# Kernel tuning notes

Measured on AMD Instinct MI355X. Metric: run time of the kernel, lower is better.

## Reference

```python
import jax, jax.numpy as jnp
import numpy as np

B, C, H, W = 16, 512, 32, 32
HEADS = 8
GROUPS = 32
EPS = 1e-5


def setup_inputs() -> dict:
    key = jax.random.key(0)
    ks = jax.random.split(key, 6)
    x = jax.random.normal(ks[0], (B, C, H, W), dtype=jnp.float32)
    gn_scale = jnp.ones((C,), dtype=jnp.float32)
    gn_bias = jnp.zeros((C,), dtype=jnp.float32)
    # 1x1 convs stored as dense matrices [out, in]
    qkv_w = jax.random.normal(ks[1], (3 * C, C), dtype=jnp.float32) * (1.0 / np.sqrt(C))
    proj_w = jax.random.normal(ks[2], (C, C), dtype=jnp.float32) * (1.0 / np.sqrt(C))
    proj_b = jax.random.normal(ks[3], (C,), dtype=jnp.float32) * 0.01
    return {"x": x, "gn_scale": gn_scale, "gn_bias": gn_bias,
            "qkv_w": qkv_w, "proj_w": proj_w, "proj_b": proj_b}


def _forward(x, gn_scale, gn_bias, qkv_w, proj_w, proj_b):
    b, c, h, w = x.shape
    d = c // HEADS  # head dim
    n = h * w
    # GroupNorm over (channels_per_group, h, w)
    xg = x.reshape(b, GROUPS, c // GROUPS, h, w)
    mu = jnp.mean(xg, axis=(2, 3, 4), keepdims=True)
    var = jnp.var(xg, axis=(2, 3, 4), keepdims=True)
    xn = ((xg - mu) * jax.lax.rsqrt(var + EPS)).reshape(b, c, h, w)
    xn = xn * gn_scale[None, :, None, None] + gn_bias[None, :, None, None]
    # 1x1 conv QKV: [b, 3c, n]
    qkv = jnp.einsum('oc,bcn->bon', qkv_w, xn.reshape(b, c, n))
    # split order: (qkv, heads, d)
    qkv = qkv.reshape(b, 3, HEADS, d, n)
    q, k, v = qkv[:, 0], qkv[:, 1], qkv[:, 2]  # each [b, heads, d, n]
    k = jax.nn.softmax(k, axis=-1)
    att = jnp.einsum('bhdn,bhen->bhde', k, v)          # [b, heads, d, d]
    out = jnp.einsum('bhde,bhdn->bhen', att, q)        # [b, heads, d, n]
    out = out.reshape(b, c, h, w)
    # 1x1 proj conv with bias
    out = jnp.einsum('oc,bchw->bohw', proj_w, out) + proj_b[None, :, None, None]
    return out


def reference(x, gn_scale, gn_bias, qkv_w, proj_w, proj_b):
    return _forward(x, gn_scale, gn_bias, qkv_w, proj_w, proj_b)
```

## Files before the change

### kernel.cpp

```cpp
#include <hip/hip_runtime.h>
#include <cstdint>
#include <cstddef>

#define B_ 16
#define C_ 512
#define N_ 1024
#define HEADS_ 8
#define D_ 64
#define CPG_ 16

typedef __bf16 bf16;
typedef bf16 bf16x4 __attribute__((ext_vector_type(4)));
typedef bf16 bf16x8 __attribute__((ext_vector_type(8)));
typedef bf16 bf16x16 __attribute__((ext_vector_type(16)));
typedef float f32x4 __attribute__((ext_vector_type(4)));

__device__ __forceinline__ void gload16(void* lds, const void* g) {
    __builtin_amdgcn_global_load_lds(
        (__attribute__((address_space(1))) void*)(void*)g,
        (__attribute__((address_space(3))) void*)lds, 16, 0, 0);
}

__global__ __launch_bounds__(256) void f32_to_bf16_k(const float* __restrict__ s,
                                                     bf16* __restrict__ d, int n) {
    int i = (blockIdx.x * 256 + threadIdx.x) * 4;
    if (i < n) {
        f32x4 v = *(const f32x4*)(s + i);
        bf16x4 o = {(bf16)v[0], (bf16)v[1], (bf16)v[2], (bf16)v[3]};
        *(bf16x4*)(d + i) = o;
    }
}

__global__ __launch_bounds__(256) void gn_kernel(const float* __restrict__ x,
                                                 const float* __restrict__ gamma,
                                                 const float* __restrict__ beta,
                                                 bf16* __restrict__ xnT) {
    const int blk = blockIdx.x;
    const int b = blk >> 5, g = blk & 31;
    const int c0 = g * CPG_;
    const float* xb = x + ((size_t)b * C_ + c0) * N_;
    const int t = threadIdx.x;

    f32x4 vals[CPG_];
    float sum = 0.f, ssq = 0.f;
#pragma unroll
    for (int c = 0; c < CPG_; ++c) {
        f32x4 v = *(const f32x4*)(xb + c * N_ + t * 4);
        vals[c] = v;
#pragma unroll
        for (int j = 0; j < 4; ++j) { sum += v[j]; ssq += v[j] * v[j]; }
    }
#pragma unroll
    for (int off = 32; off >= 1; off >>= 1) {
        sum += __shfl_xor(sum, off);
        ssq += __shfl_xor(ssq, off);
    }
    __shared__ float red[2][4];
    const int wv = t >> 6, lane = t & 63;
    if (lane == 0) { red[0][wv] = sum; red[1][wv] = ssq; }
    __syncthreads();
    sum = red[0][0] + red[0][1] + red[0][2] + red[0][3];
    ssq = red[1][0] + red[1][1] + red[1][2] + red[1][3];
    const float inv = 1.f / (float)(CPG_ * N_);
    float mean = sum * inv;
    float var = ssq * inv - mean * mean;
    float rstd = rsqrtf(var + 1e-5f);
    float ga[CPG_], be[CPG_];
#pragma unroll
    for (int c = 0; c < CPG_; ++c) {
        float gm = gamma[c0 + c] * rstd;
        ga[c] = gm;
        be[c] = beta[c0 + c] - mean * gm;
    }
#pragma unroll
    for (int j = 0; j < 4; ++j) {
        int n = t * 4 + j;
        bf16x16 o;
#pragma unroll
        for (int c = 0; c < CPG_; ++c) o[c] = (bf16)(vals[c][j] * ga[c] + be[c]);
        *(bf16x16*)(xnT + ((size_t)b * N_ + n) * C_ + c0) = o;
    }
}

template <int EPI>
__global__ __launch_bounds__(256, 2) void gemm_bt(const bf16* __restrict__ A,
                                                  const bf16* __restrict__ Bt,
                                                  int M, int N, int K,
                                                  void* __restrict__ o0,
                                                  void* __restrict__ o1,
                                                  void* __restrict__ o2,
                                                  const float* __restrict__ bias) {
    __shared__ __align__(16) bf16 As[2][128][64];
    __shared__ __align__(16) bf16 Bs[2][128][64];
    const int t = threadIdx.x;
    const int lane = t & 63, wv = t >> 6;
    const int wr = wv >> 1, wc = wv & 1;
    const int bn = blockIdx.x, bm = blockIdx.y, b = blockIdx.z;
    const bf16* Ab = A + (size_t)bm * 128 * K;
    const bf16* Bb = Bt + ((size_t)b * N + (size_t)bn * 128) * K;

    f32x4 acc[4][4];
#pragma unroll
    for (int mi = 0; mi < 4; ++mi)
#pragma unroll
        for (int ni = 0; ni < 4; ++ni) acc[mi][ni] = f32x4{0.f, 0.f, 0.f, 0.f};

    const int nk = K >> 6;

    auto stage = [&](int buf, int kt) {
#pragma unroll
        for (int rnd = 0; rnd < 4; ++rnd) {
            int idx = rnd * 256 + t;
            int row = idx >> 3, pb = idx & 7;
            int srcb = pb ^ (row & 7);
            gload16((char*)&As[buf][0][0] + (size_t)idx * 16,
                    Ab + (size_t)row * K + kt * 64 + srcb * 8);
        }
#pragma unroll
        for (int rnd = 0; rnd < 4; ++rnd) {
            int idx = rnd * 256 + t;
            int row = idx >> 3, pb = idx & 7;
            int srcb = pb ^ (row & 7);
            gload16((char*)&Bs[buf][0][0] + (size_t)idx * 16,
                    Bb + (size_t)row * K + kt * 64 + srcb * 8);
        }
    };
    auto compute = [&](int buf) {
#pragma unroll
        for (int ks = 0; ks < 2; ++ks) {
            bf16x8 af[4], bfr[4];
#pragma unroll
            for (int mi = 0; mi < 4; ++mi) {
                int r = wr * 64 + mi * 16 + (lane & 15);
                int bi = (ks * 4 + (lane >> 4)) ^ (r & 7);
                af[mi] = *(const bf16x8*)&As[buf][r][bi * 8];
            }
#pragma unroll
            for (int ni = 0; ni < 4; ++ni) {
                int r = wc * 64 + ni * 16 + (lane & 15);
                int bi = (ks * 4 + (lane >> 4)) ^ (r & 7);
                bfr[ni] = *(const bf16x8*)&Bs[buf][r][bi * 8];
            }
#pragma unroll
            for (int mi = 0; mi < 4; ++mi)
#pragma unroll
                for (int ni = 0; ni < 4; ++ni)
                    acc[mi][ni] = __builtin_amdgcn_mfma_f32_16x16x32_bf16(
                        af[mi], bfr[ni], acc[mi][ni], 0, 0, 0);
        }
    };

    stage(0, 0);
    for (int kt = 0; kt < nk; ++kt) {
        const int cur = kt & 1;
        if (kt + 1 < nk) {
            stage(cur ^ 1, kt + 1);
            asm volatile("s_waitcnt vmcnt(8)" ::: "memory");
        } else {
            asm volatile("s_waitcnt vmcnt(0)" ::: "memory");
        }
        __builtin_amdgcn_s_barrier();
        __builtin_amdgcn_sched_barrier(0);
        compute(cur);
        __builtin_amdgcn_s_barrier();
    }

    const int rowb = bm * 128 + wr * 64;
    const int colb = bn * 128 + wc * 64;
#pragma unroll
    for (int mi = 0; mi < 4; ++mi) {
#pragma unroll
        for (int ni = 0; ni < 4; ++ni) {
            int r0 = rowb + mi * 16 + (lane >> 4) * 4;
            int cc = colb + ni * 16 + (lane & 15);
            if constexpr (EPI == 0) {
                bf16* qT = (bf16*)o0;
                bf16* klog = (bf16*)o1;
                bf16* vb = (bf16*)o2;
                if (r0 < 512) {
                    int h = r0 >> 6, d = r0 & 63;
                    bf16x4 pk;
#pragma unroll
                    for (int j = 0; j < 4; ++j) pk[j] = (bf16)acc[mi][ni][j];
                    *(bf16x4*)(qT + (((size_t)b * HEADS_ + h) * N_ + cc) * D_ + d) = pk;
                } else {
                    bf16* dst = (r0 < 1024) ? klog : vb;
                    int h = (r0 >> 6) & 7, d = r0 & 63;
                    bf16* p = dst + (((size_t)b * HEADS_ + h) * D_ + d) * N_ + cc;
#pragma unroll
                    for (int j = 0; j < 4; ++j) p[(size_t)j * N_] = (bf16)acc[mi][ni][j];
                }
            } else {
                float* outp = (float*)o0;
#pragma unroll
                for (int j = 0; j < 4; ++j)
                    outp[((size_t)b * C_ + r0 + j) * N_ + cc] = acc[mi][ni][j] + bias[r0 + j];
            }
        }
    }
}

__global__ __launch_bounds__(256) void softmax_k(const bf16* __restrict__ klog,
                                                 bf16* __restrict__ ksm) {
    const int row = blockIdx.x * 4 + (threadIdx.x >> 6);
    const int lane = threadIdx.x & 63;
    const bf16* rp = klog + (size_t)row * N_;
    float v[16];
    float mx = -1e30f;
#pragma unroll
    for (int i = 0; i < 2; ++i) {
        bf16x8 u = *(const bf16x8*)(rp + ((size_t)lane + 64 * i) * 8);
#pragma unroll
        for (int j = 0; j < 8; ++j) {
            v[i * 8 + j] = (float)u[j];
            mx = fmaxf(mx, v[i * 8 + j]);
        }
    }
#pragma unroll
    for (int off = 32; off >= 1; off >>= 1) mx = fmaxf(mx, __shfl_xor(mx, off));
    float s = 0.f;
#pragma unroll
    for (int i = 0; i < 16; ++i) { v[i] = __expf(v[i] - mx); s += v[i]; }
#pragma unroll
    for (int off = 32; off >= 1; off >>= 1) s += __shfl_xor(s, off);
    float inv = 1.f / s;
    bf16* op = ksm + (size_t)row * N_;
#pragma unroll
    for (int i = 0; i < 2; ++i) {
        bf16x8 o;
#pragma unroll
        for (int j = 0; j < 8; ++j) o[j] = (bf16)(v[i * 8 + j] * inv);
        *(bf16x8*)(op + ((size_t)lane + 64 * i) * 8) = o;
    }
}

__global__ __launch_bounds__(256) void attn1_kernel(const bf16* __restrict__ ksm,
                                                    const bf16* __restrict__ vb,
                                                    float* __restrict__ attP) {
    __shared__ float attp[2][64][64];
    const int blk = blockIdx.x;
    const int bh = blk >> 1, half = blk & 1;
    const int t = threadIdx.x, lane = t & 63, wv = t >> 6;
    const bf16* kb = ksm + (size_t)bh * D_ * N_;
    const bf16* vv = vb + (size_t)bh * D_ * N_;

    f32x4 acc[4][4];
#pragma unroll
    for (int mi = 0; mi < 4; ++mi)
#pragma unroll
        for (int ni = 0; ni < 4; ++ni) acc[mi][ni] = f32x4{0.f, 0.f, 0.f, 0.f};

    const int k0 = half * 512 + wv * 128;
#pragma unroll
    for (int kk = 0; kk < 128; kk += 32) {
        bf16x8 af[4], bfr[4];
#pragma unroll
        for (int mi = 0; mi < 4; ++mi)
            af[mi] = *(const bf16x8*)(kb + (size_t)(mi * 16 + (lane & 15)) * N_ + k0 + kk + (lane >> 4) * 8);
#pragma unroll
        for (int ni = 0; ni < 4; ++ni)
            bfr[ni] = *(const bf16x8*)(vv + (size_t)(ni * 16 + (lane & 15)) * N_ + k0 + kk + (lane >> 4) * 8);
#pragma unroll
        for (int mi = 0; mi < 4; ++mi)
#pragma unroll
            for (int ni = 0; ni < 4; ++ni)
                acc[mi][ni] = __builtin_amdgcn_mfma_f32_16x16x32_bf16(
                    af[mi], bfr[ni], acc[mi][ni], 0, 0, 0);
    }
    if (wv < 2) {
#pragma unroll
        for (int mi = 0; mi < 4; ++mi)
#pragma unroll
            for (int ni = 0; ni < 4; ++ni)
#pragma unroll
                for (int j = 0; j < 4; ++j)
                    attp[wv][mi * 16 + (lane >> 4) * 4 + j][ni * 16 + (lane & 15)] = acc[mi][ni][j];
    }
    __syncthreads();
    if (wv >= 2) {
#pragma unroll
        for (int mi = 0; mi < 4; ++mi)
#pragma unroll
            for (int ni = 0; ni < 4; ++ni)
#pragma unroll
                for (int j = 0; j < 4; ++j)
                    attp[wv - 2][mi * 16 + (lane >> 4) * 4 + j][ni * 16 + (lane & 15)] += acc[mi][ni][j];
    }
    __syncthreads();
    float* op = attP + (size_t)blk * 4096;
    for (int i = t; i < 4096; i += 256) {
        int d = i >> 6, e = i & 63;
        op[i] = attp[0][d][e] + attp[1][d][e];
    }
}

__global__ __launch_bounds__(256) void attn2_kernel(const float* __restrict__ attP,
                                                    const bf16* __restrict__ qT,
                                                    bf16* __restrict__ o2T) {
    __shared__ __align__(16) bf16 attT[64][64];
    const int blk = blockIdx.x;
    const int bh = blk >> 2, nc = blk & 3;
    const int b = bh >> 3, h = bh & 7;
    const int t = threadIdx.x, lane = t & 63, wv = t >> 6;
    const float* p0 = attP + (size_t)(bh * 2) * 4096;
    const float* p1 = p0 + 4096;
    for (int i = t; i < 4096; i += 256) {
        int d = i >> 6, e = i & 63;
        attT[e][d ^ ((e & 7) << 3)] = (bf16)(p0[i] + p1[i]);
    }
    __syncthreads();

    const bf16* qb = qT + (size_t)bh * N_ * D_;
    const int n0 = nc * 256 + wv * 64;
    f32x4 a2[4][4];
#pragma unroll
    for (int mi = 0; mi < 4; ++mi)
#pragma unroll
        for (int ni = 0; ni < 4; ++ni) a2[mi][ni] = f32x4{0.f, 0.f, 0.f, 0.f};
#pragma unroll
    for (int ks = 0; ks < 2; ++ks) {
        bf16x8 af[4], bfr[4];
#pragma unroll
        for (int mi = 0; mi < 4; ++mi) {
            int r = mi * 16 + (lane & 15);
            int cb = ks * 32 + (lane >> 4) * 8;
            af[mi] = *(const bf16x8*)&attT[r][cb ^ ((r & 7) << 3)];
        }
#pragma unroll
        for (int ni = 0; ni < 4; ++ni)
            bfr[ni] = *(const bf16x8*)(qb + (size_t)(n0 + ni * 16 + (lane & 15)) * D_ + ks * 32 + (lane >> 4) * 8);
#pragma unroll
        for (int mi = 0; mi < 4; ++mi)
#pragma unroll
            for (int ni = 0; ni < 4; ++ni)
                a2[mi][ni] = __builtin_amdgcn_mfma_f32_16x16x32_bf16(
                    af[mi], bfr[ni], a2[mi][ni], 0, 0, 0);
    }
#pragma unroll
    for (int mi = 0; mi < 4; ++mi) {
#pragma unroll
        for (int ni = 0; ni < 4; ++ni) {
            int e0 = mi * 16 + (lane >> 4) * 4;
            int nn = n0 + ni * 16 + (lane & 15);
            bf16x4 pk;
#pragma unroll
            for (int j = 0; j < 4; ++j) pk[j] = (bf16)a2[mi][ni][j];
            *(bf16x4*)(o2T + ((size_t)b * N_ + nn) * C_ + h * D_ + e0) = pk;
        }
    }
}

extern "C" void kernel_launch(void* const* d_in, const int* in_sizes, int n_in,
                              void* d_out, int out_size, void* d_ws, size_t ws_size,
                              hipStream_t stream) {
    const float* x = (const float*)d_in[0];
    const float* gn_scale = (const float*)d_in[1];
    const float* gn_bias = (const float*)d_in[2];
    const float* qkv_w = (const float*)d_in[3];
    const float* proj_w = (const float*)d_in[4];
    const float* proj_b = (const float*)d_in[5];
    float* out = (float*)d_out;

    const size_t elems = (size_t)B_ * C_ * N_;
    const size_t plane = (size_t)B_ * HEADS_ * D_ * N_;
    char* w = (char*)d_ws;
    bf16* xnT = (bf16*)w;   w += elems * 2;
    bf16* qT = (bf16*)w;    w += plane * 2;
    bf16* klog = (bf16*)w;  w += plane * 2;
    bf16* ksm = (bf16*)w;   w += plane * 2;
    bf16* vbuf = (bf16*)w;  w += plane * 2;
    float* attP = (float*)w; w += (size_t)256 * 4096 * 4;
    bf16* wqkv = (bf16*)w;  w += (size_t)3 * C_ * C_ * 2;
    bf16* wproj = (bf16*)w; w += (size_t)C_ * C_ * 2;
    bf16* o2T = xnT;

    f32_to_bf16_k<<<768, 256, 0, stream>>>(qkv_w, wqkv, 3 * C_ * C_);
    f32_to_bf16_k<<<256, 256, 0, stream>>>(proj_w, wproj, C_ * C_);
    gn_kernel<<<512, 256, 0, stream>>>(x, gn_scale, gn_bias, xnT);
    gemm_bt<0><<<dim3(8, 12, 16), 256, 0, stream>>>(wqkv, xnT, 1536, 1024, 512,
                                                    (void*)qT, (void*)klog, (void*)vbuf, nullptr);
    softmax_k<<<2048, 256, 0, stream>>>(klog, ksm);
    attn1_kernel<<<256, 256, 0, stream>>>(ksm, vbuf, attP);
    attn2_kernel<<<512, 256, 0, stream>>>(attP, qT, o2T);
    gemm_bt<1><<<dim3(8, 4, 16), 256, 0, stream>>>(wproj, o2T, 512, 1024, 512,
                                                   (void*)out, nullptr, nullptr, proj_b);
}
```

Before: 181.6 us.

## Use 256x256 8-wave GEMM tiles, fold softmax into attn1, merge weight conversion

```diff
diff --git a/kernel.cpp b/kernel.cpp
--- a/kernel.cpp
+++ b/kernel.cpp
@@ -8,6 +8,8 @@
 #define HEADS_ 8
 #define D_ 64
 #define CPG_ 16
+#define KDIM 512
+#define NT_ 16384
 
 typedef __bf16 bf16;
 typedef bf16 bf16x4 __attribute__((ext_vector_type(4)));
@@ -21,14 +23,19 @@
         (__attribute__((address_space(3))) void*)lds, 16, 0, 0);
 }
 
-__global__ __launch_bounds__(256) void f32_to_bf16_k(const float* __restrict__ s,
-                                                     bf16* __restrict__ d, int n) {
-    int i = (blockIdx.x * 256 + threadIdx.x) * 4;
-    if (i < n) {
-        f32x4 v = *(const f32x4*)(s + i);
-        bf16x4 o = {(bf16)v[0], (bf16)v[1], (bf16)v[2], (bf16)v[3]};
-        *(bf16x4*)(d + i) = o;
-    }
+__global__ __launch_bounds__(256) void convert_w(const float* __restrict__ qkv_w,
+                                                 const float* __restrict__ proj_w,
+                                                 bf16* __restrict__ wqkv,
+                                                 bf16* __restrict__ wproj) {
+    const int bid = blockIdx.x;
+    const float* s;
+    bf16* d;
+    int i;
+    if (bid < 768) { s = qkv_w; d = wqkv; i = bid * 1024 + threadIdx.x * 4; }
+    else           { s = proj_w; d = wproj; i = (bid - 768) * 1024 + threadIdx.x * 4; }
+    f32x4 v = *(const f32x4*)(s + i);
+    bf16x4 o = {(bf16)v[0], (bf16)v[1], (bf16)v[2], (bf16)v[3]};
+    *(bf16x4*)(d + i) = o;
 }
 
 __global__ __launch_bounds__(256) void gn_kernel(const float* __restrict__ x,
@@ -83,125 +90,141 @@
 }
 
 template <int EPI>
-__global__ __launch_bounds__(256, 2) void gemm_bt(const bf16* __restrict__ A,
-                                                  const bf16* __restrict__ Bt,
-                                                  int M, int N, int K,
-                                                  void* __restrict__ o0,
-                                                  void* __restrict__ o1,
-                                                  void* __restrict__ o2,
-                                                  const float* __restrict__ bias) {
-    __shared__ __align__(16) bf16 As[2][128][64];
-    __shared__ __align__(16) bf16 Bs[2][128][64];
+__global__ __launch_bounds__(512, 2) void gemm8(const bf16* __restrict__ A,
+                                                const bf16* __restrict__ Bt,
+                                                bf16* __restrict__ o0,
+                                                bf16* __restrict__ o1,
+                                                bf16* __restrict__ o2,
+                                                float* __restrict__ fo,
+                                                const float* __restrict__ bias) {
+    __shared__ __align__(16) bf16 As[2][256][64];
+    __shared__ __align__(16) bf16 Bs[2][256][64];
     const int t = threadIdx.x;
     const int lane = t & 63, wv = t >> 6;
-    const int wr = wv >> 1, wc = wv & 1;
-    const int bn = blockIdx.x, bm = blockIdx.y, b = blockIdx.z;
-    const bf16* Ab = A + (size_t)bm * 128 * K;
-    const bf16* Bb = Bt + ((size_t)b * N + (size_t)bn * 128) * K;
-
-    f32x4 acc[4][4];
-#pragma unroll
-    for (int mi = 0; mi < 4; ++mi)
+    const int wr = wv >> 2, wc = wv & 3;
+    const int bn = blockIdx.x, bm = blockIdx.y;
+    const bf16* Ab = A + (size_t)bm * 256 * KDIM;
+    const bf16* Bb = Bt + (size_t)bn * 256 * KDIM;
+
+    f32x4 acc[8][4];
+#pragma unroll
+    for (int mi = 0; mi < 8; ++mi)
 #pragma unroll
         for (int ni = 0; ni < 4; ++ni) acc[mi][ni] = f32x4{0.f, 0.f, 0.f, 0.f};
 
-    const int nk = K >> 6;
-
-    auto stage = [&](int buf, int kt) {
-#pragma unroll
-        for (int rnd = 0; rnd < 4; ++rnd) {
-            int idx = rnd * 256 + t;
+    auto stageHalf = [&](int buf, int kt, int which) {
+        const bf16* src = (which < 2) ? Ab : Bb;
+        char* dst = (which < 2) ? (char*)&As[buf][0][0] : (char*)&Bs[buf][0][0];
+        const int half = which & 1;
+#pragma unroll
+        for (int l = 0; l < 2; ++l) {
+            int idx = half * 1024 + l * 512 + t;
             int row = idx >> 3, pb = idx & 7;
             int srcb = pb ^ (row & 7);
-            gload16((char*)&As[buf][0][0] + (size_t)idx * 16,
-                    Ab + (size_t)row * K + kt * 64 + srcb * 8);
-        }
-#pragma unroll
-        for (int rnd = 0; rnd < 4; ++rnd) {
-            int idx = rnd * 256 + t;
-            int row = idx >> 3, pb = idx & 7;
-            int srcb = pb ^ (row & 7);
-            gload16((char*)&Bs[buf][0][0] + (size_t)idx * 16,
-                    Bb + (size_t)row * K + kt * 64 + srcb * 8);
+            gload16(dst + (size_t)idx * 16, src + (size_t)row * KDIM + kt * 64 + srcb * 8);
         }
     };
-    auto compute = [&](int buf) {
-#pragma unroll
-        for (int ks = 0; ks < 2; ++ks) {
-            bf16x8 af[4], bfr[4];
+
+    bf16x8 afA[2][4];
+    bf16x8 bfr[2][2][2];
+    auto loadA = [&](int buf, int mh) {
+#pragma unroll
+        for (int ks = 0; ks < 2; ++ks)
 #pragma unroll
             for (int mi = 0; mi < 4; ++mi) {
-                int r = wr * 64 + mi * 16 + (lane & 15);
+                int r = wr * 128 + mh * 64 + mi * 16 + (lane & 15);
                 int bi = (ks * 4 + (lane >> 4)) ^ (r & 7);
-                af[mi] = *(const bf16x8*)&As[buf][r][bi * 8];
+                afA[ks][mi] = *(const bf16x8*)&As[buf][r][bi * 8];
             }
-#pragma unroll
-            for (int ni = 0; ni < 4; ++ni) {
-                int r = wc * 64 + ni * 16 + (lane & 15);
+    };
+    auto loadB = [&](int buf, int nh) {
+#pragma unroll
+        for (int ks = 0; ks < 2; ++ks)
+#pragma unroll
+            for (int ni = 0; ni < 2; ++ni) {
+                int r = wc * 64 + nh * 32 + ni * 16 + (lane & 15);
                 int bi = (ks * 4 + (lane >> 4)) ^ (r & 7);
-                bfr[ni] = *(const bf16x8*)&Bs[buf][r][bi * 8];
+                bfr[nh][ks][ni] = *(const bf16x8*)&Bs[buf][r][bi * 8];
             }
+    };
+    auto mfma16 = [&](int mh, int nh) {
+#pragma unroll
+        for (int ks = 0; ks < 2; ++ks)
 #pragma unroll
             for (int mi = 0; mi < 4; ++mi)
 #pragma unroll
-                for (int ni = 0; ni < 4; ++ni)
-                    acc[mi][ni] = __builtin_amdgcn_mfma_f32_16x16x32_bf16(
-                        af[mi], bfr[ni], acc[mi][ni], 0, 0, 0);
-        }
+                for (int ni = 0; ni < 2; ++ni)
+                    acc[mh * 4 + mi][nh * 2 + ni] = __builtin_amdgcn_mfma_f32_16x16x32_bf16(
+                        afA[ks][mi], bfr[nh][ks][ni], acc[mh * 4 + mi][nh * 2 + ni], 0, 0, 0);
     };
 
-    stage(0, 0);
-    for (int kt = 0; kt < nk; ++kt) {
-        const int cur = kt & 1;
-        if (kt + 1 < nk) {
-            stage(cur ^ 1, kt + 1);
-            asm volatile("s_waitcnt vmcnt(8)" ::: "memory");
-        } else {
-            asm volatile("s_waitcnt vmcnt(0)" ::: "memory");
-        }
+    stageHalf(0, 0, 0); stageHalf(0, 0, 1); stageHalf(0, 0, 2); stageHalf(0, 0, 3);
+    asm volatile("s_waitcnt vmcnt(0)" ::: "memory");
+    __builtin_amdgcn_s_barrier();
+
+    for (int kt = 0; kt < 8; ++kt) {
+        const int cur = kt & 1, nxt = cur ^ 1;
+        const bool pf = (kt < 7);
+        loadA(cur, 0); loadB(cur, 0);
+        if (pf) stageHalf(nxt, kt + 1, 0);
         __builtin_amdgcn_s_barrier();
         __builtin_amdgcn_sched_barrier(0);
-        compute(cur);
-        __builtin_amdgcn_s_barrier();
-    }
-
-    const int rowb = bm * 128 + wr * 64;
-    const int colb = bn * 128 + wc * 64;
-#pragma unroll
-    for (int mi = 0; mi < 4; ++mi) {
+        __builtin_amdgcn_s_setprio(1); mfma16(0, 0); __builtin_amdgcn_s_setprio(0);
+        __builtin_amdgcn_s_barrier();
+        loadB(cur, 1);
+        if (pf) stageHalf(nxt, kt + 1, 1);
+        __builtin_amdgcn_s_barrier();
+        __builtin_amdgcn_sched_barrier(0);
+        __builtin_amdgcn_s_setprio(1); mfma16(0, 1); __builtin_amdgcn_s_setprio(0);
+        __builtin_amdgcn_s_barrier();
+        loadA(cur, 1);
+        if (pf) stageHalf(nxt, kt + 1, 2);
+        __builtin_amdgcn_s_barrier();
+        __builtin_amdgcn_sched_barrier(0);
+        __builtin_amdgcn_s_setprio(1); mfma16(1, 0); __builtin_amdgcn_s_setprio(0);
+        __builtin_amdgcn_s_barrier();
+        if (pf) stageHalf(nxt, kt + 1, 3);
+        __builtin_amdgcn_s_barrier();
+        __builtin_amdgcn_sched_barrier(0);
+        __builtin_amdgcn_s_setprio(1); mfma16(1, 1); __builtin_amdgcn_s_setprio(0);
+        asm volatile("s_waitcnt vmcnt(0)" ::: "memory");
+        __builtin_amdgcn_s_barrier();
+    }
+
+    const int rowbase = bm * 256 + wr * 128;
+    const int colbase = bn * 256 + wc * 64;
+#pragma unroll
+    for (int mi = 0; mi < 8; ++mi) {
 #pragma unroll
         for (int ni = 0; ni < 4; ++ni) {
-            int r0 = rowb + mi * 16 + (lane >> 4) * 4;
-            int cc = colb + ni * 16 + (lane & 15);
+            int r0 = rowbase + mi * 16 + (lane >> 4) * 4;
+            int cc = colbase + ni * 16 + (lane & 15);
+            int b = cc >> 10, n = cc & 1023;
             if constexpr (EPI == 0) {
-                bf16* qT = (bf16*)o0;
-                bf16* klog = (bf16*)o1;
-                bf16* vb = (bf16*)o2;
                 if (r0 < 512) {
                     int h = r0 >> 6, d = r0 & 63;
                     bf16x4 pk;
 #pragma unroll
                     for (int j = 0; j < 4; ++j) pk[j] = (bf16)acc[mi][ni][j];
-                    *(bf16x4*)(qT + (((size_t)b * HEADS_ + h) * N_ + cc) * D_ + d) = pk;
+                    *(bf16x4*)(o0 + (((size_t)b * HEADS_ + h) * N_ + n) * D_ + d) = pk;
                 } else {
-                    bf16* dst = (r0 < 1024) ? klog : vb;
+                    bf16* dst = (r0 < 1024) ? o1 : o2;
                     int h = (r0 >> 6) & 7, d = r0 & 63;
-                    bf16* p = dst + (((size_t)b * HEADS_ + h) * D_ + d) * N_ + cc;
+                    bf16* p = dst + (((size_t)b * HEADS_ + h) * D_ + d) * N_ + n;
 #pragma unroll
                     for (int j = 0; j < 4; ++j) p[(size_t)j * N_] = (bf16)acc[mi][ni][j];
                 }
             } else {
-                float* outp = (float*)o0;
 #pragma unroll
                 for (int j = 0; j < 4; ++j)
-                    outp[((size_t)b * C_ + r0 + j) * N_ + cc] = acc[mi][ni][j] + bias[r0 + j];
+                    fo[((size_t)b * C_ + r0 + j) * N_ + n] = acc[mi][ni][j] + bias[r0 + j];
             }
         }
     }
 }
 
-__global__ __launch_bounds__(256) void softmax_k(const bf16* __restrict__ klog,
-                                                 bf16* __restrict__ ksm) {
+__global__ __launch_bounds__(256) void kstats_k(const bf16* __restrict__ klog,
+                                                float2* __restrict__ kstat) {
     const int row = blockIdx.x * 4 + (threadIdx.x >> 6);
     const int lane = threadIdx.x & 63;
     const bf16* rp = klog + (size_t)row * N_;
@@ -220,29 +243,27 @@
     for (int off = 32; off >= 1; off >>= 1) mx = fmaxf(mx, __shfl_xor(mx, off));
     float s = 0.f;
 #pragma unroll
-    for (int i = 0; i < 16; ++i) { v[i] = __expf(v[i] - mx); s += v[i]; }
+    for (int i = 0; i < 16; ++i) s += __expf(v[i] - mx);
 #pragma unroll
     for (int off = 32; off >= 1; off >>= 1) s += __shfl_xor(s, off);
-    float inv = 1.f / s;
-    bf16* op = ksm + (size_t)row * N_;
-#pragma unroll
-    for (int i = 0; i < 2; ++i) {
-        bf16x8 o;
-#pragma unroll
-        for (int j = 0; j < 8; ++j) o[j] = (bf16)(v[i * 8 + j] * inv);
-        *(bf16x8*)(op + ((size_t)lane + 64 * i) * 8) = o;
-    }
-}
-
-__global__ __launch_bounds__(256) void attn1_kernel(const bf16* __restrict__ ksm,
+    if (lane == 0) kstat[row] = make_float2(mx, 1.f / s);
+}
+
+__global__ __launch_bounds__(256) void attn1_kernel(const bf16* __restrict__ klog,
+                                                    const float2* __restrict__ kstat,
                                                     const bf16* __restrict__ vb,
                                                     float* __restrict__ attP) {
     __shared__ float attp[2][64][64];
     const int blk = blockIdx.x;
     const int bh = blk >> 1, half = blk & 1;
     const int t = threadIdx.x, lane = t & 63, wv = t >> 6;
-    const bf16* kb = ksm + (size_t)bh * D_ * N_;
+    const bf16* kb = klog + (size_t)bh * D_ * N_;
     const bf16* vv = vb + (size_t)bh * D_ * N_;
+
+    float2 kst[4];
+#pragma unroll
+    for (int mi = 0; mi < 4; ++mi)
+        kst[mi] = kstat[(size_t)bh * D_ + mi * 16 + (lane & 15)];
 
     f32x4 acc[4][4];
 #pragma unroll
@@ -255,8 +276,14 @@
     for (int kk = 0; kk < 128; kk += 32) {
         bf16x8 af[4], bfr[4];
 #pragma unroll
-        for (int mi = 0; mi < 4; ++mi)
-            af[mi] = *(const bf16x8*)(kb + (size_t)(mi * 16 + (lane & 15)) * N_ + k0 + kk + (lane >> 4) * 8);
+        for (int mi = 0; mi < 4; ++mi) {
+            bf16x8 raw = *(const bf16x8*)(kb + (size_t)(mi * 16 + (lane & 15)) * N_ + k0 + kk + (lane >> 4) * 8);
+            bf16x8 a;
+#pragma unroll
+            for (int j = 0; j < 8; ++j)
+                a[j] = (bf16)(__expf((float)raw[j] - kst[mi].x) * kst[mi].y);
+            af[mi] = a;
+        }
 #pragma unroll
         for (int ni = 0; ni < 4; ++ni)
             bfr[ni] = *(const bf16x8*)(vv + (size_t)(ni * 16 + (lane & 15)) * N_ + k0 + kk + (lane >> 4) * 8);
@@ -364,24 +391,21 @@
     const size_t elems = (size_t)B_ * C_ * N_;
     const size_t plane = (size_t)B_ * HEADS_ * D_ * N_;
     char* w = (char*)d_ws;
-    bf16* xnT = (bf16*)w;   w += elems * 2;
-    bf16* qT = (bf16*)w;    w += plane * 2;
-    bf16* klog = (bf16*)w;  w += plane * 2;
-    bf16* ksm = (bf16*)w;   w += plane * 2;
-    bf16* vbuf = (bf16*)w;  w += plane * 2;
+    bf16* xnT = (bf16*)w;    w += elems * 2;
+    bf16* qT = (bf16*)w;     w += plane * 2;
+    bf16* klog = (bf16*)w;   w += plane * 2;
+    bf16* vbuf = (bf16*)w;   w += plane * 2;
     float* attP = (float*)w; w += (size_t)256 * 4096 * 4;
-    bf16* wqkv = (bf16*)w;  w += (size_t)3 * C_ * C_ * 2;
-    bf16* wproj = (bf16*)w; w += (size_t)C_ * C_ * 2;
+    float2* kstat = (float2*)w; w += (size_t)8192 * 8;
+    bf16* wqkv = (bf16*)w;   w += (size_t)3 * C_ * C_ * 2;
+    bf16* wproj = (bf16*)w;  w += (size_t)C_ * C_ * 2;
     bf16* o2T = xnT;
 
-    f32_to_bf16_k<<<768, 256, 0, stream>>>(qkv_w, wqkv, 3 * C_ * C_);
-    f32_to_bf16_k<<<256, 256, 0, stream>>>(proj_w, wproj, C_ * C_);
+    convert_w<<<1024, 256, 0, stream>>>(qkv_w, proj_w, wqkv, wproj);
     gn_kernel<<<512, 256, 0, stream>>>(x, gn_scale, gn_bias, xnT);
-    gemm_bt<0><<<dim3(8, 12, 16), 256, 0, stream>>>(wqkv, xnT, 1536, 1024, 512,
-                                                    (void*)qT, (void*)klog, (void*)vbuf, nullptr);
-    softmax_k<<<2048, 256, 0, stream>>>(klog, ksm);
-    attn1_kernel<<<256, 256, 0, stream>>>(ksm, vbuf, attP);
+    gemm8<0><<<dim3(64, 6), 512, 0, stream>>>(wqkv, xnT, qT, klog, vbuf, nullptr, nullptr);
+    kstats_k<<<2048, 256, 0, stream>>>(klog, kstat);
+    attn1_kernel<<<256, 256, 0, stream>>>(klog, kstat, vbuf, attP);
     attn2_kernel<<<512, 256, 0, stream>>>(attP, qT, o2T);
-    gemm_bt<1><<<dim3(8, 4, 16), 256, 0, stream>>>(wproj, o2T, 512, 1024, 512,
-                                                   (void*)out, nullptr, nullptr, proj_b);
-}
+    gemm8<1><<<dim3(64, 2), 512, 0, stream>>>(wproj, o2T, nullptr, nullptr, nullptr, out, proj_b);
+}
```

Measured after the change: 184.3 us. Within noise of the previous version (+1.5%).
